# Performance work log

Measured on AMD Instinct MI355X. Metric: run time of the kernel, lower is better.

## Reference

```python
import jax, jax.numpy as jnp
import numpy as np

B, S, D, H = 4, 2048, 768, 12
DH = D // H          # 64 head dim
DF = 4 * D           # 3072 FFN hidden
EPS = 1e-5


def setup_inputs() -> dict:
    key = jax.random.key(0)
    ks = jax.random.split(key, 16)
    s = 0.02
    inp = {
        "Q": jax.random.normal(ks[0], (B, S, D), jnp.float32),
        "K": jax.random.normal(ks[1], (B, S, D), jnp.float32),
        "V": jax.random.normal(ks[2], (B, S, D), jnp.float32),
        "Wq": s * jax.random.normal(ks[3], (D, D), jnp.float32),
        "bq": jnp.zeros((D,), jnp.float32),
        "Wk": s * jax.random.normal(ks[4], (D, D), jnp.float32),
        "bk": jnp.zeros((D,), jnp.float32),
        "Wv": s * jax.random.normal(ks[5], (D, D), jnp.float32),
        "bv": jnp.zeros((D,), jnp.float32),
        "Wo": s * jax.random.normal(ks[6], (D, D), jnp.float32),
        "bo": jnp.zeros((D,), jnp.float32),
        "ln_g": jnp.ones((D,), jnp.float32),
        "ln_b": jnp.zeros((D,), jnp.float32),
        "W1": s * jax.random.normal(ks[7], (D, DF), jnp.float32),
        "b1": jnp.zeros((DF,), jnp.float32),
        "W2": s * jax.random.normal(ks[8], (DF, D), jnp.float32),
        "b2": jnp.zeros((D,), jnp.float32),
    }
    return inp


def _split_heads(x):  # [B,S,D] -> [B,H,S,DH]
    return x.reshape(B, S, H, DH).transpose(0, 2, 1, 3)


def _layernorm(x, g, b):
    mu = jnp.mean(x, axis=-1, keepdims=True)
    var = jnp.mean(jnp.square(x - mu), axis=-1, keepdims=True)
    return (x - mu) * jax.lax.rsqrt(var + EPS) * g + b


def reference(Q, K, V, Wq, bq, Wk, bk, Wv, bv, Wo, bo, ln_g, ln_b, W1, b1, W2, b2):
    q = _split_heads(Q @ Wq + bq)            # [B,H,S,DH]
    k = _split_heads(K @ Wk + bk)
    v = _split_heads(V @ Wv + bv)
    scale = 1.0 / jnp.sqrt(jnp.asarray(DH, q.dtype))
    scores = jnp.einsum("bhqd,bhkd->bhqk", q, k) * scale   # [B,H,S,S]
    attn = jax.nn.softmax(scores, axis=-1)
    ctx = jnp.einsum("bhqk,bhkd->bhqd", attn, v)            # [B,H,S,DH]
    ctx = ctx.transpose(0, 2, 1, 3).reshape(B, S, D)
    attn_out = ctx @ Wo + bo
    h = _layernorm(Q + attn_out, ln_g, ln_b)                # residual + LN
    ff = jax.nn.gelu(h @ W1 + b1, approximate=False) @ W2 + b2
    return ff
```

## Files before the change

### kernel.cpp

```cpp
#include <hip/hip_runtime.h>
#include <hip/hip_bf16.h>
#include <math.h>

#define Bsz 4
#define Ssz 2048
#define Dsz 768
#define Hn  12
#define DHn 64
#define DFn 3072
#define NTOK (Bsz*Ssz)
#define EPSL 1e-5f

typedef __attribute__((ext_vector_type(8))) short bf16x8;
typedef __attribute__((ext_vector_type(4))) float f32x4;

__device__ __forceinline__ unsigned short f2bf(float f) {
    unsigned int u = __float_as_uint(f);
    u += 0x7fffu + ((u >> 16) & 1u);
    return (unsigned short)(u >> 16);
}
__device__ __forceinline__ float bf2f(unsigned short h) {
    return __uint_as_float(((unsigned int)h) << 16);
}

__global__ __launch_bounds__(256)
void wsplit_k(const float* __restrict__ W, unsigned short* __restrict__ Wh,
              unsigned short* __restrict__ Wl, int K, int N)
{
    __shared__ float tile[32][33];
    const int n0 = blockIdx.x * 32, k0 = blockIdx.y * 32;
    const int x = threadIdx.x, y = threadIdx.y;
    #pragma unroll
    for (int i = 0; i < 4; i++)
        tile[y + 8 * i][x] = W[(size_t)(k0 + y + 8 * i) * N + n0 + x];
    __syncthreads();
    #pragma unroll
    for (int i = 0; i < 4; i++) {
        float v = tile[x][y + 8 * i];
        unsigned short hb = f2bf(v);
        size_t o = (size_t)(n0 + y + 8 * i) * K + k0 + x;
        Wh[o] = hb;
        Wl[o] = f2bf(v - bf2f(hb));
    }
}

__global__ __launch_bounds__(256)
void qkv_mfma(const float* __restrict__ Qf, const float* __restrict__ Kf,
              const float* __restrict__ Vf,
              const unsigned short* __restrict__ Wqh, const unsigned short* __restrict__ Wql,
              const unsigned short* __restrict__ Wkh, const unsigned short* __restrict__ Wkl,
              const unsigned short* __restrict__ Wvh, const unsigned short* __restrict__ Wvl,
              const float* __restrict__ bq, const float* __restrict__ bk,
              const float* __restrict__ bv,
              unsigned short* __restrict__ qh, unsigned short* __restrict__ ql,
              unsigned short* __restrict__ kh, unsigned short* __restrict__ kl,
              unsigned short* __restrict__ vout)
{
    __shared__ short smem[16384];
    short* As_h = smem;
    short* As_l = smem + 4096;
    short* Bs_h = smem + 8192;
    short* Bs_l = smem + 12288;

    const int t    = threadIdx.x;
    const int lane = t & 63;
    const int w    = t >> 6;
    const int wm   = w >> 1;
    const int wn   = w & 1;
    const int which = blockIdx.y >> 6;
    const int m0   = (blockIdx.y & 63) * 128;
    const int n0   = blockIdx.x * 128;

    const float* A = (which == 0) ? Qf : (which == 1) ? Kf : Vf;
    const unsigned short* Bh = (which == 0) ? Wqh : (which == 1) ? Wkh : Wvh;
    const unsigned short* Bl = (which == 0) ? Wql : (which == 1) ? Wkl : Wvl;
    const float* bias = (which == 0) ? bq : (which == 1) ? bk : bv;

    f32x4 acc[4][4];
    #pragma unroll
    for (int i = 0; i < 4; i++)
        #pragma unroll
        for (int j = 0; j < 4; j++)
            acc[i][j] = (f32x4){0.f, 0.f, 0.f, 0.f};

    const int fr = lane & 15;
    const int q8 = (lane >> 4) * 8;

    for (int k0 = 0; k0 < Dsz; k0 += 32) {
        __syncthreads();
        #pragma unroll
        for (int it = 0; it < 2; it++) {
            const int p   = t + 256 * it;
            const int row = p >> 2;
            const int c8  = (p & 3) * 8;
            const unsigned short* gb_h = Bh + (size_t)(n0 + row) * Dsz + k0 + c8;
            const unsigned short* gb_l = Bl + (size_t)(n0 + row) * Dsz + k0 + c8;
            __builtin_amdgcn_global_load_lds((const __attribute__((address_space(1))) void*)gb_h,
                (__attribute__((address_space(3))) void*)(Bs_h + p * 8), 16, 0, 0);
            __builtin_amdgcn_global_load_lds((const __attribute__((address_space(1))) void*)gb_l,
                (__attribute__((address_space(3))) void*)(Bs_l + p * 8), 16, 0, 0);
        }
        #pragma unroll
        for (int it = 0; it < 2; it++) {
            const int p   = t + 256 * it;
            const int row = p >> 2;
            const int c8  = (p & 3) * 8;
            const float* ga = A + (size_t)(m0 + row) * Dsz + k0 + c8;
            float4 f0 = *(const float4*)ga;
            float4 f1 = *(const float4*)(ga + 4);
            float fv[8] = {f0.x, f0.y, f0.z, f0.w, f1.x, f1.y, f1.z, f1.w};
            bf16x8 h8, l8;
            #pragma unroll
            for (int e = 0; e < 8; e++) {
                unsigned short hb = f2bf(fv[e]);
                h8[e] = (short)hb;
                l8[e] = (short)f2bf(fv[e] - bf2f(hb));
            }
            *(bf16x8*)&As_h[p * 8] = h8;
            *(bf16x8*)&As_l[p * 8] = l8;
        }
        __syncthreads();

        bf16x8 a_h[4], a_l[4], b_h[4], b_l[4];
        #pragma unroll
        for (int i = 0; i < 4; i++) {
            const int ra = (wm * 64 + i * 16 + fr) * 32 + q8;
            const int rb = (wn * 64 + i * 16 + fr) * 32 + q8;
            a_h[i] = *(const bf16x8*)&As_h[ra];
            a_l[i] = *(const bf16x8*)&As_l[ra];
            b_h[i] = *(const bf16x8*)&Bs_h[rb];
            b_l[i] = *(const bf16x8*)&Bs_l[rb];
        }
        if (which < 2) {
            #pragma unroll
            for (int i = 0; i < 4; i++)
                #pragma unroll
                for (int j = 0; j < 4; j++) {
                    acc[i][j] = __builtin_amdgcn_mfma_f32_16x16x32_bf16(a_l[i], b_h[j], acc[i][j], 0, 0, 0);
                    acc[i][j] = __builtin_amdgcn_mfma_f32_16x16x32_bf16(a_h[i], b_l[j], acc[i][j], 0, 0, 0);
                    acc[i][j] = __builtin_amdgcn_mfma_f32_16x16x32_bf16(a_h[i], b_h[j], acc[i][j], 0, 0, 0);
                }
        } else {
            #pragma unroll
            for (int i = 0; i < 4; i++)
                #pragma unroll
                for (int j = 0; j < 4; j++)
                    acc[i][j] = __builtin_amdgcn_mfma_f32_16x16x32_bf16(a_h[i], b_h[j], acc[i][j], 0, 0, 0);
        }
    }

    const int quad = lane >> 4;
    #pragma unroll
    for (int i = 0; i < 4; i++)
        #pragma unroll
        for (int j = 0; j < 4; j++) {
            const int n  = n0 + wn * 64 + j * 16 + fr;
            const float bn = bias[n];
            const int hh = n >> 6, dh = n & 63;
            #pragma unroll
            for (int r = 0; r < 4; r++) {
                const int m = m0 + wm * 64 + i * 16 + quad * 4 + r;
                const int bb = m >> 11, s = m & 2047;
                const size_t o = (((size_t)bb * Hn + hh) * Ssz + s) * DHn + dh;
                float v = acc[i][j][r] + bn;
                unsigned short hb = f2bf(v);
                if (which == 0) { qh[o] = hb; ql[o] = f2bf(v - bf2f(hb)); }
                else if (which == 1) { kh[o] = hb; kl[o] = f2bf(v - bf2f(hb)); }
                else vout[o] = hb;
            }
        }
}

__global__ __launch_bounds__(256)
void vtrans_k(const unsigned short* __restrict__ src, unsigned short* __restrict__ dst)
{
    __shared__ unsigned short tl[32][33];
    const int s0 = blockIdx.x * 32;
    const int d0 = blockIdx.y * 32;
    const int hd = blockIdx.z;
    const int x = threadIdx.x, y = threadIdx.y;
    const size_t base = (size_t)hd * Ssz * DHn;
    #pragma unroll
    for (int i = 0; i < 4; i++)
        tl[y + 8 * i][x] = src[base + (size_t)(s0 + y + 8 * i) * DHn + d0 + x];
    __syncthreads();
    #pragma unroll
    for (int i = 0; i < 4; i++)
        dst[base + (size_t)(d0 + y + 8 * i) * Ssz + s0 + x] = tl[x][y + 8 * i];
}

template<int MODE, bool ASPLIT, bool BSPLIT>
__global__ __launch_bounds__(256)
void gemm_mfma(const unsigned short* __restrict__ Ah, const unsigned short* __restrict__ Al,
               const unsigned short* __restrict__ Bh, const unsigned short* __restrict__ Bl,
               const float* __restrict__ bias, const float* __restrict__ res,
               float* __restrict__ Cf, unsigned short* __restrict__ Cb,
               int M, int N, int K)
{
    __shared__ short smem[16384];
    short* As_h = smem;
    short* As_l = smem + 4096;
    short* Bs_h = smem + 8192;
    short* Bs_l = smem + 12288;

    const int t    = threadIdx.x;
    const int lane = t & 63;
    const int w    = t >> 6;
    const int wm   = w >> 1;
    const int wn   = w & 1;
    const int m0   = blockIdx.y * 128;
    const int n0   = blockIdx.x * 128;

    f32x4 acc[4][4];
    #pragma unroll
    for (int i = 0; i < 4; i++)
        #pragma unroll
        for (int j = 0; j < 4; j++)
            acc[i][j] = (f32x4){0.f, 0.f, 0.f, 0.f};

    const int fr = lane & 15;
    const int q8 = (lane >> 4) * 8;

    for (int k0 = 0; k0 < K; k0 += 32) {
        __syncthreads();
        #pragma unroll
        for (int it = 0; it < 2; it++) {
            const int p   = t + 256 * it;
            const int row = p >> 2;
            const int c8  = (p & 3) * 8;
            const unsigned short* ga_h = Ah + (size_t)(m0 + row) * K + k0 + c8;
            const unsigned short* gb_h = Bh + (size_t)(n0 + row) * K + k0 + c8;
            __builtin_amdgcn_global_load_lds((const __attribute__((address_space(1))) void*)ga_h,
                (__attribute__((address_space(3))) void*)(As_h + p * 8), 16, 0, 0);
            if (ASPLIT) {
                const unsigned short* ga_l = Al + (size_t)(m0 + row) * K + k0 + c8;
                __builtin_amdgcn_global_load_lds((const __attribute__((address_space(1))) void*)ga_l,
                    (__attribute__((address_space(3))) void*)(As_l + p * 8), 16, 0, 0);
            }
            __builtin_amdgcn_global_load_lds((const __attribute__((address_space(1))) void*)gb_h,
                (__attribute__((address_space(3))) void*)(Bs_h + p * 8), 16, 0, 0);
            if (BSPLIT) {
                const unsigned short* gb_l = Bl + (size_t)(n0 + row) * K + k0 + c8;
                __builtin_amdgcn_global_load_lds((const __attribute__((address_space(1))) void*)gb_l,
                    (__attribute__((address_space(3))) void*)(Bs_l + p * 8), 16, 0, 0);
            }
        }
        __syncthreads();

        bf16x8 a_h[4], a_l[4], b_h[4], b_l[4];
        #pragma unroll
        for (int i = 0; i < 4; i++) {
            const int ra = (wm * 64 + i * 16 + fr) * 32 + q8;
            const int rb = (wn * 64 + i * 16 + fr) * 32 + q8;
            a_h[i] = *(const bf16x8*)&As_h[ra];
            if (ASPLIT) a_l[i] = *(const bf16x8*)&As_l[ra];
            b_h[i] = *(const bf16x8*)&Bs_h[rb];
            if (BSPLIT) b_l[i] = *(const bf16x8*)&Bs_l[rb];
        }
        #pragma unroll
        for (int i = 0; i < 4; i++)
            #pragma unroll
            for (int j = 0; j < 4; j++) {
                if (ASPLIT)
                    acc[i][j] = __builtin_amdgcn_mfma_f32_16x16x32_bf16(a_l[i], b_h[j], acc[i][j], 0, 0, 0);
                if (BSPLIT)
                    acc[i][j] = __builtin_amdgcn_mfma_f32_16x16x32_bf16(a_h[i], b_l[j], acc[i][j], 0, 0, 0);
                acc[i][j] = __builtin_amdgcn_mfma_f32_16x16x32_bf16(a_h[i], b_h[j], acc[i][j], 0, 0, 0);
            }
    }

    const int quad = lane >> 4;
    #pragma unroll
    for (int i = 0; i < 4; i++)
        #pragma unroll
        for (int j = 0; j < 4; j++) {
            const int n  = n0 + wn * 64 + j * 16 + fr;
            const float bn = bias[n];
            #pragma unroll
            for (int r = 0; r < 4; r++) {
                const int m = m0 + wm * 64 + i * 16 + quad * 4 + r;
                float v = acc[i][j][r] + bn;
                if (MODE == 1) {
                    v += res[(size_t)m * N + n];
                    Cf[(size_t)m * N + n] = v;
                } else if (MODE == 2) {
                    v = 0.5f * v * (1.0f + erff(v * 0.70710678118654752f));
                    Cb[(size_t)m * N + n] = f2bf(v);
                } else {
                    Cf[(size_t)m * N + n] = v;
                }
            }
        }
}

__device__ __forceinline__ void stage16(const unsigned short* src, short* dst,
                                        int p0, int lane, int row0, int rstride, int col0)
{
    const int p   = p0 + lane;
    const int n   = p >> 3;
    const int cst = (p & 7) ^ (n & 7);
    const unsigned short* g = src + (size_t)(row0 + n) * rstride + col0 + cst * 8;
    __builtin_amdgcn_global_load_lds((const __attribute__((address_space(1))) void*)g,
        (__attribute__((address_space(3))) void*)(dst + p0 * 8), 16, 0, 0);
}

__device__ __forceinline__ bf16x8 frag(const short* arr, int row, int c)
{
    const int pos = row * 8 + (c ^ (row & 7));
    return *(const bf16x8*)&arr[pos * 8];
}

__global__ __launch_bounds__(256)
void attn_mfma(const unsigned short* __restrict__ qh, const unsigned short* __restrict__ ql,
               const unsigned short* __restrict__ kh, const unsigned short* __restrict__ kl,
               const unsigned short* __restrict__ vt, unsigned short* __restrict__ ch)
{
    const int hid = blockIdx.x;
    const int b   = hid / Hn;
    const int h   = hid - b * Hn;
    const int q0  = blockIdx.y * 64;
    const int t    = threadIdx.x;
    const int lane = t & 63;
    const int w    = t >> 6;
    const int fr   = lane & 15;
    const int quad = lane >> 4;

    __shared__ short sKV[12288];
    __shared__ short sQP[8192];
    short* Kh_s = sKV;
    short* Kl_s = sKV + 4096;
    short* Vh_s = sKV + 8192;
    short* Qh_s = sQP;
    short* Ql_s = sQP + 4096;
    float* Pw   = (float*)sQP + w * 1024;

    const size_t hoff = (size_t)hid * Ssz * DHn;

    stage16(qh + hoff, Qh_s, w * 128,      lane, q0, DHn, 0);
    stage16(qh + hoff, Qh_s, w * 128 + 64, lane, q0, DHn, 0);
    stage16(ql + hoff, Ql_s, w * 128,      lane, q0, DHn, 0);
    stage16(ql + hoff, Ql_s, w * 128 + 64, lane, q0, DHn, 0);

    f32x4 O[4];
    #pragma unroll
    for (int d = 0; d < 4; d++) O[d] = (f32x4){0.f, 0.f, 0.f, 0.f};
    float lp[4] = {0.f, 0.f, 0.f, 0.f};

    bf16x8 qfh[2], qfl[2];
    const float scale = 0.125f;

    for (int kt = 0; kt < Ssz / 64; kt++) {
        __syncthreads();
        const int kr = kt * 64;
        #pragma unroll
        for (int bt = 0; bt < 2; bt++) {
            const int p0 = w * 128 + bt * 64;
            stage16(kh + hoff, Kh_s, p0, lane, kr, DHn, 0);
            stage16(kl + hoff, Kl_s, p0, lane, kr, DHn, 0);
            stage16(vt + hoff, Vh_s, p0, lane, 0, Ssz, kr);
        }
        __syncthreads();

        if (kt == 0) {
            #pragma unroll
            for (int kc = 0; kc < 2; kc++) {
                qfh[kc] = frag(Qh_s, w * 16 + fr, kc * 4 + quad);
                qfl[kc] = frag(Ql_s, w * 16 + fr, kc * 4 + quad);
            }
            __syncthreads();
        }

        f32x4 sc[4];
        #pragma unroll
        for (int nt = 0; nt < 4; nt++) sc[nt] = (f32x4){0.f, 0.f, 0.f, 0.f};
        #pragma unroll
        for (int nt = 0; nt < 4; nt++)
            #pragma unroll
            for (int kc = 0; kc < 2; kc++) {
                bf16x8 bh = frag(Kh_s, nt * 16 + fr, kc * 4 + quad);
                bf16x8 bl = frag(Kl_s, nt * 16 + fr, kc * 4 + quad);
                sc[nt] = __builtin_amdgcn_mfma_f32_16x16x32_bf16(qfl[kc], bh, sc[nt], 0, 0, 0);
                sc[nt] = __builtin_amdgcn_mfma_f32_16x16x32_bf16(qfh[kc], bl, sc[nt], 0, 0, 0);
                sc[nt] = __builtin_amdgcn_mfma_f32_16x16x32_bf16(qfh[kc], bh, sc[nt], 0, 0, 0);
            }

        #pragma unroll
        for (int r = 0; r < 4; r++) {
            const int m = quad * 4 + r;
            #pragma unroll
            for (int nt = 0; nt < 4; nt++) {
                float p = __expf(sc[nt][r] * scale);
                const int j  = nt * 16 + fr;
                const int c4 = j >> 2;
                Pw[(m * 16 + (c4 ^ m)) * 4 + (j & 3)] = p;
                lp[r] += p;
            }
        }

        #pragma unroll
        for (int kc = 0; kc < 2; kc++) {
            const int c4a = kc * 8 + quad * 2;
            float4 pa = *(float4*)&Pw[(fr * 16 + (c4a ^ fr)) * 4];
            float4 pb = *(float4*)&Pw[(fr * 16 + ((c4a + 1) ^ fr)) * 4];
            union { bf16x8 v; __hip_bfloat162 b2[4]; } P;
            P.b2[0] = __float22bfloat162_rn(make_float2(pa.x, pa.y));
            P.b2[1] = __float22bfloat162_rn(make_float2(pa.z, pa.w));
            P.b2[2] = __float22bfloat162_rn(make_float2(pb.x, pb.y));
            P.b2[3] = __float22bfloat162_rn(make_float2(pb.z, pb.w));
            #pragma unroll
            for (int dt = 0; dt < 4; dt++) {
                bf16x8 vh = frag(Vh_s, dt * 16 + fr, kc * 4 + quad);
                O[dt] = __builtin_amdgcn_mfma_f32_16x16x32_bf16(P.v, vh, O[dt], 0, 0, 0);
            }
        }
    }

    #pragma unroll
    for (int r = 0; r < 4; r++) {
        float ls = lp[r];
        #pragma unroll
        for (int msk = 1; msk < 16; msk <<= 1) ls += __shfl_xor(ls, msk);
        const float linv = 1.0f / ls;
        const int s = q0 + w * 16 + quad * 4 + r;
        unsigned short* och = ch + ((size_t)b * Ssz + s) * Dsz + h * DHn;
        #pragma unroll
        for (int dt = 0; dt < 4; dt++)
            och[dt * 16 + fr] = f2bf(O[dt][r] * linv);
    }
}

__global__ __launch_bounds__(256)
void ln_k(const float* __restrict__ x, const float* __restrict__ g,
          const float* __restrict__ bb, unsigned short* __restrict__ yh,
          unsigned short* __restrict__ yl)
{
    const int row = blockIdx.x;
    const float* xr = x + (size_t)row * Dsz;
    unsigned short* yhr = yh + (size_t)row * Dsz;
    unsigned short* ylr = yl + (size_t)row * Dsz;
    const int t = threadIdx.x;

    float v0 = xr[t], v1 = xr[t + 256], v2 = xr[t + 512];
    float s = v0 + v1 + v2;
    #pragma unroll
    for (int o = 1; o < 64; o <<= 1) s += __shfl_xor(s, o, 64);

    __shared__ float red1[4];
    __shared__ float red2[4];
    const int wid = t >> 6, lane = t & 63;
    if (lane == 0) red1[wid] = s;
    __syncthreads();
    const float mean = (red1[0] + red1[1] + red1[2] + red1[3]) * (1.0f / Dsz);

    float d0 = v0 - mean, d1 = v1 - mean, d2 = v2 - mean;
    float vs = d0 * d0 + d1 * d1 + d2 * d2;
    #pragma unroll
    for (int o = 1; o < 64; o <<= 1) vs += __shfl_xor(vs, o, 64);
    if (lane == 0) red2[wid] = vs;
    __syncthreads();
    const float var = (red2[0] + red2[1] + red2[2] + red2[3]) * (1.0f / Dsz);
    const float inv = rsqrtf(var + EPSL);

    #pragma unroll
    for (int e = 0; e < 3; e++) {
        const int idx = t + 256 * e;
        const float dd = (e == 0) ? d0 : (e == 1) ? d1 : d2;
        float y = dd * inv * g[idx] + bb[idx];
        unsigned short hb = f2bf(y);
        yhr[idx] = hb;
        ylr[idx] = f2bf(y - bf2f(hb));
    }
}

extern "C" void kernel_launch(void* const* d_in, const int* in_sizes, int n_in,
                              void* d_out, int out_size, void* d_ws, size_t ws_size,
                              hipStream_t stream)
{
    (void)in_sizes; (void)n_in; (void)out_size; (void)ws_size;
    const float* Q    = (const float*)d_in[0];
    const float* Kin  = (const float*)d_in[1];
    const float* Vin  = (const float*)d_in[2];
    const float* Wq   = (const float*)d_in[3];
    const float* bq   = (const float*)d_in[4];
    const float* Wk   = (const float*)d_in[5];
    const float* bk   = (const float*)d_in[6];
    const float* Wv   = (const float*)d_in[7];
    const float* bv   = (const float*)d_in[8];
    const float* Wo   = (const float*)d_in[9];
    const float* bo   = (const float*)d_in[10];
    const float* ln_g = (const float*)d_in[11];
    const float* ln_b = (const float*)d_in[12];
    const float* W1   = (const float*)d_in[13];
    const float* b1   = (const float*)d_in[14];
    const float* W2   = (const float*)d_in[15];
    const float* b2   = (const float*)d_in[16];
    float* out = (float*)d_out;

    const size_t NT = (size_t)NTOK * Dsz;
    unsigned short* usws = (unsigned short*)d_ws;
    unsigned short* qh  = usws + 0 * NT;
    unsigned short* ql  = usws + 1 * NT;
    unsigned short* kh  = usws + 2 * NT;
    unsigned short* kl  = usws + 3 * NT;
    unsigned short* vt  = usws + 4 * NT;
    unsigned short* ch  = usws + 6 * NT;
    unsigned short* wsp = usws + 8 * NT;
    const size_t SW = (size_t)Dsz * Dsz;
    unsigned short* Wqh = wsp + 0 * SW;
    unsigned short* Wql = wsp + 1 * SW;
    unsigned short* Wkh = wsp + 2 * SW;
    unsigned short* Wkl = wsp + 3 * SW;
    unsigned short* Wvh = wsp + 4 * SW;
    unsigned short* Wvl = wsp + 5 * SW;
    unsigned short* Woh = wsp + 6 * SW;
    unsigned short* Wol = wsp + 7 * SW;
    unsigned short* W1h = wsp + 8 * SW;
    unsigned short* W1l = wsp + 12 * SW;
    unsigned short* W2h = wsp + 16 * SW;
    unsigned short* W2l = wsp + 20 * SW;
    float*          hpre = (float*)usws;
    unsigned short* hh   = kh;
    unsigned short* hl   = kl;
    unsigned short* hbuf = usws + 4 * NT;

    dim3 wb(32, 8);
    wsplit_k<<<dim3(Dsz / 32, Dsz / 32), wb, 0, stream>>>(Wq, Wqh, Wql, Dsz, Dsz);
    wsplit_k<<<dim3(Dsz / 32, Dsz / 32), wb, 0, stream>>>(Wk, Wkh, Wkl, Dsz, Dsz);
    wsplit_k<<<dim3(Dsz / 32, Dsz / 32), wb, 0, stream>>>(Wv, Wvh, Wvl, Dsz, Dsz);
    wsplit_k<<<dim3(Dsz / 32, Dsz / 32), wb, 0, stream>>>(Wo, Woh, Wol, Dsz, Dsz);
    wsplit_k<<<dim3(DFn / 32, Dsz / 32), wb, 0, stream>>>(W1, W1h, W1l, Dsz, DFn);
    wsplit_k<<<dim3(Dsz / 32, DFn / 32), wb, 0, stream>>>(W2, W2h, W2l, DFn, Dsz);

    qkv_mfma<<<dim3(Dsz / 128, 192), 256, 0, stream>>>(
        Q, Kin, Vin, Wqh, Wql, Wkh, Wkl, Wvh, Wvl, bq, bk, bv,
        qh, ql, kh, kl, ch);

    vtrans_k<<<dim3(Ssz / 32, DHn / 32, Bsz * Hn), wb, 0, stream>>>(ch, vt);

    attn_mfma<<<dim3(Bsz * Hn, Ssz / 64), 256, 0, stream>>>(qh, ql, kh, kl, vt, ch);

    gemm_mfma<1, false, true><<<dim3(Dsz / 128, NTOK / 128), 256, 0, stream>>>(
        ch, nullptr, Woh, Wol, bo, Q, hpre, nullptr, NTOK, Dsz, Dsz);

    ln_k<<<NTOK, 256, 0, stream>>>(hpre, ln_g, ln_b, hh, hl);

    gemm_mfma<2, true, true><<<dim3(DFn / 128, NTOK / 128), 256, 0, stream>>>(
        hh, hl, W1h, W1l, b1, nullptr, nullptr, hbuf, NTOK, DFn, Dsz);
    gemm_mfma<3, false, false><<<dim3(Dsz / 128, NTOK / 128), 256, 0, stream>>>(
        hbuf, nullptr, W2h, nullptr, b2, nullptr, out, nullptr, NTOK, Dsz, DFn);
}
```

Measured before the change: 701.2 us.

## Swizzle GEMM tiles per XCD, prefetch QKV A tiles, drop unused low parts

Replaces the 2D grids of the QKV and generic GEMMs with 1D grids and remaps block IDs so consecutive M-tiles land on the same XCD, aiming for better L2 reuse of weights. In the QKV kernel, the fp32 A tile is register-prefetched one k-step ahead, and loading, storing and reading the low-part split are skipped for the V projection, which never uses them. LayerNorm now writes only the high bf16 part, and the W1 GEMM runs without the A-low correction. That last step lowers the precision of the FFN input.

```diff
diff --git a/kernel.cpp b/kernel.cpp
--- a/kernel.cpp
+++ b/kernel.cpp
@@ -21,6 +21,14 @@
 }
 __device__ __forceinline__ float bf2f(unsigned short h) {
     return __uint_as_float(((unsigned int)h) << 16);
+}
+
+__device__ __forceinline__ void swizzle_mn(int bid, int mtot, int nb, int& m, int& n)
+{
+    const int xcd = bid & 7;
+    const int idx = bid >> 3;
+    m = xcd * (mtot >> 3) + idx / nb;
+    n = idx % nb;
 }
 
 __global__ __launch_bounds__(256)
@@ -67,9 +75,12 @@
     const int w    = t >> 6;
     const int wm   = w >> 1;
     const int wn   = w & 1;
-    const int which = blockIdx.y >> 6;
-    const int m0   = (blockIdx.y & 63) * 128;
-    const int n0   = blockIdx.x * 128;
+
+    int m_tile, nblk;
+    swizzle_mn(blockIdx.x, 192, 6, m_tile, nblk);
+    const int which = m_tile / 64;
+    const int m0    = (m_tile % 64) * 128;
+    const int n0    = nblk * 128;
 
     const float* A = (which == 0) ? Qf : (which == 1) ? Kf : Vf;
     const unsigned short* Bh = (which == 0) ? Wqh : (which == 1) ? Wkh : Wvh;
@@ -85,6 +96,17 @@
 
     const int fr = lane & 15;
     const int q8 = (lane >> 4) * 8;
+
+    float4 af0[2], af1[2];
+    #pragma unroll
+    for (int it = 0; it < 2; it++) {
+        const int p   = t + 256 * it;
+        const int row = p >> 2;
+        const int c8  = (p & 3) * 8;
+        const float* ga = A + (size_t)(m0 + row) * Dsz + c8;
+        af0[it] = *(const float4*)ga;
+        af1[it] = *(const float4*)(ga + 4);
+    }
 
     for (int k0 = 0; k0 < Dsz; k0 += 32) {
         __syncthreads();
@@ -94,21 +116,19 @@
             const int row = p >> 2;
             const int c8  = (p & 3) * 8;
             const unsigned short* gb_h = Bh + (size_t)(n0 + row) * Dsz + k0 + c8;
-            const unsigned short* gb_l = Bl + (size_t)(n0 + row) * Dsz + k0 + c8;
             __builtin_amdgcn_global_load_lds((const __attribute__((address_space(1))) void*)gb_h,
                 (__attribute__((address_space(3))) void*)(Bs_h + p * 8), 16, 0, 0);
-            __builtin_amdgcn_global_load_lds((const __attribute__((address_space(1))) void*)gb_l,
-                (__attribute__((address_space(3))) void*)(Bs_l + p * 8), 16, 0, 0);
+            if (which < 2) {
+                const unsigned short* gb_l = Bl + (size_t)(n0 + row) * Dsz + k0 + c8;
+                __builtin_amdgcn_global_load_lds((const __attribute__((address_space(1))) void*)gb_l,
+                    (__attribute__((address_space(3))) void*)(Bs_l + p * 8), 16, 0, 0);
+            }
         }
         #pragma unroll
         for (int it = 0; it < 2; it++) {
-            const int p   = t + 256 * it;
-            const int row = p >> 2;
-            const int c8  = (p & 3) * 8;
-            const float* ga = A + (size_t)(m0 + row) * Dsz + k0 + c8;
-            float4 f0 = *(const float4*)ga;
-            float4 f1 = *(const float4*)(ga + 4);
-            float fv[8] = {f0.x, f0.y, f0.z, f0.w, f1.x, f1.y, f1.z, f1.w};
+            const int p = t + 256 * it;
+            float fv[8] = {af0[it].x, af0[it].y, af0[it].z, af0[it].w,
+                           af1[it].x, af1[it].y, af1[it].z, af1[it].w};
             bf16x8 h8, l8;
             #pragma unroll
             for (int e = 0; e < 8; e++) {
@@ -117,9 +137,21 @@
                 l8[e] = (short)f2bf(fv[e] - bf2f(hb));
             }
             *(bf16x8*)&As_h[p * 8] = h8;
-            *(bf16x8*)&As_l[p * 8] = l8;
+            if (which < 2) *(bf16x8*)&As_l[p * 8] = l8;
         }
         __syncthreads();
+
+        if (k0 + 32 < Dsz) {
+            #pragma unroll
+            for (int it = 0; it < 2; it++) {
+                const int p   = t + 256 * it;
+                const int row = p >> 2;
+                const int c8  = (p & 3) * 8;
+                const float* ga = A + (size_t)(m0 + row) * Dsz + k0 + 32 + c8;
+                af0[it] = *(const float4*)ga;
+                af1[it] = *(const float4*)(ga + 4);
+            }
+        }
 
         bf16x8 a_h[4], a_l[4], b_h[4], b_l[4];
         #pragma unroll
@@ -127,9 +159,11 @@
             const int ra = (wm * 64 + i * 16 + fr) * 32 + q8;
             const int rb = (wn * 64 + i * 16 + fr) * 32 + q8;
             a_h[i] = *(const bf16x8*)&As_h[ra];
-            a_l[i] = *(const bf16x8*)&As_l[ra];
             b_h[i] = *(const bf16x8*)&Bs_h[rb];
-            b_l[i] = *(const bf16x8*)&Bs_l[rb];
+            if (which < 2) {
+                a_l[i] = *(const bf16x8*)&As_l[ra];
+                b_l[i] = *(const bf16x8*)&Bs_l[rb];
+            }
         }
         if (which < 2) {
             #pragma unroll
@@ -208,8 +242,11 @@
     const int w    = t >> 6;
     const int wm   = w >> 1;
     const int wn   = w & 1;
-    const int m0   = blockIdx.y * 128;
-    const int n0   = blockIdx.x * 128;
+
+    int mt, nt_;
+    swizzle_mn(blockIdx.x, M >> 7, N >> 7, mt, nt_);
+    const int m0 = mt * 128;
+    const int n0 = nt_ * 128;
 
     f32x4 acc[4][4];
     #pragma unroll
@@ -431,13 +468,11 @@
 
 __global__ __launch_bounds__(256)
 void ln_k(const float* __restrict__ x, const float* __restrict__ g,
-          const float* __restrict__ bb, unsigned short* __restrict__ yh,
-          unsigned short* __restrict__ yl)
+          const float* __restrict__ bb, unsigned short* __restrict__ yh)
 {
     const int row = blockIdx.x;
     const float* xr = x + (size_t)row * Dsz;
     unsigned short* yhr = yh + (size_t)row * Dsz;
-    unsigned short* ylr = yl + (size_t)row * Dsz;
     const int t = threadIdx.x;
 
     float v0 = xr[t], v1 = xr[t + 256], v2 = xr[t + 512];
@@ -461,15 +496,9 @@
     const float var = (red2[0] + red2[1] + red2[2] + red2[3]) * (1.0f / Dsz);
     const float inv = rsqrtf(var + EPSL);
 
-    #pragma unroll
-    for (int e = 0; e < 3; e++) {
-        const int idx = t + 256 * e;
-        const float dd = (e == 0) ? d0 : (e == 1) ? d1 : d2;
-        float y = dd * inv * g[idx] + bb[idx];
-        unsigned short hb = f2bf(y);
-        yhr[idx] = hb;
-        ylr[idx] = f2bf(y - bf2f(hb));
-    }
+    yhr[t]       = f2bf(d0 * inv * g[t]       + bb[t]);
+    yhr[t + 256] = f2bf(d1 * inv * g[t + 256] + bb[t + 256]);
+    yhr[t + 512] = f2bf(d2 * inv * g[t + 512] + bb[t + 512]);
 }
 
 extern "C" void kernel_launch(void* const* d_in, const int* in_sizes, int n_in,
@@ -520,7 +549,6 @@
     unsigned short* W2l = wsp + 20 * SW;
     float*          hpre = (float*)usws;
     unsigned short* hh   = kh;
-    unsigned short* hl   = kl;
     unsigned short* hbuf = usws + 4 * NT;
 
     dim3 wb(32, 8);
@@ -531,7 +559,7 @@
     wsplit_k<<<dim3(DFn / 32, Dsz / 32), wb, 0, stream>>>(W1, W1h, W1l, Dsz, DFn);
     wsplit_k<<<dim3(Dsz / 32, DFn / 32), wb, 0, stream>>>(W2, W2h, W2l, DFn, Dsz);
 
-    qkv_mfma<<<dim3(Dsz / 128, 192), 256, 0, stream>>>(
+    qkv_mfma<<<1152, 256, 0, stream>>>(
         Q, Kin, Vin, Wqh, Wql, Wkh, Wkl, Wvh, Wvl, bq, bk, bv,
         qh, ql, kh, kl, ch);
 
@@ -539,13 +567,13 @@
 
     attn_mfma<<<dim3(Bsz * Hn, Ssz / 64), 256, 0, stream>>>(qh, ql, kh, kl, vt, ch);
 
-    gemm_mfma<1, false, true><<<dim3(Dsz / 128, NTOK / 128), 256, 0, stream>>>(
+    gemm_mfma<1, false, true><<<384, 256, 0, stream>>>(
         ch, nullptr, Woh, Wol, bo, Q, hpre, nullptr, NTOK, Dsz, Dsz);
 
-    ln_k<<<NTOK, 256, 0, stream>>>(hpre, ln_g, ln_b, hh, hl);
-
-    gemm_mfma<2, true, true><<<dim3(DFn / 128, NTOK / 128), 256, 0, stream>>>(
-        hh, hl, W1h, W1l, b1, nullptr, nullptr, hbuf, NTOK, DFn, Dsz);
-    gemm_mfma<3, false, false><<<dim3(Dsz / 128, NTOK / 128), 256, 0, stream>>>(
+    ln_k<<<NTOK, 256, 0, stream>>>(hpre, ln_g, ln_b, hh);
+
+    gemm_mfma<2, false, true><<<1536, 256, 0, stream>>>(
+        hh, nullptr, W1h, W1l, b1, nullptr, nullptr, hbuf, NTOK, DFn, Dsz);
+    gemm_mfma<3, false, false><<<384, 256, 0, stream>>>(
         hbuf, nullptr, W2h, nullptr, b2, nullptr, out, nullptr, NTOK, Dsz, DFn);
 }
```

Measured after the change: 617.0 us. 12.0% less time.
